# Kernel tuning notes

Measured on AMD Instinct MI355X. Metric: run time of the kernel, lower is better.

## Reference

```python
import jax, jax.numpy as jnp
import numpy as np

NUM_HEADS = 8


def _mha(x, w_in, b_in, w_out, b_out, nh=NUM_HEADS):
    # x: [B, L, H]; torch nn.MultiheadAttention (batch_first) self-attention
    B, L, H = x.shape
    dh = H // nh
    qkv = x @ w_in.T + b_in                      # [B, L, 3H]
    q, k, v = jnp.split(qkv, 3, axis=-1)
    def heads(t):
        return t.reshape(B, L, nh, dh).transpose(0, 2, 1, 3)  # [B, nh, L, dh]
    q, k, v = heads(q), heads(k), heads(v)
    scale = 1.0 / np.sqrt(dh)
    scores = jnp.einsum('bhqd,bhkd->bhqk', q * scale, k)      # [B, nh, L, L]
    attn = jax.nn.softmax(scores, axis=-1)
    out = jnp.einsum('bhqk,bhkd->bhqd', attn, v)               # [B, nh, L, dh]
    out = out.transpose(0, 2, 1, 3).reshape(B, L, H)
    return out @ w_out.T + b_out


def setup_inputs() -> dict:
    key = jax.random.key(0)
    ks = jax.random.split(key, 10)
    S, M, B, H = 64, 4, 128, 1024
    std = 0.02
    inp = {
        'hidden_states_combined': jax.random.normal(ks[0], (S, M, B, 1, H), jnp.float32),
        'mf_in_w': jax.random.normal(ks[1], (3 * H, H), jnp.float32) * std,
        'mf_in_b': jnp.zeros((3 * H,), jnp.float32),
        'mf_out_w': jax.random.normal(ks[2], (H, H), jnp.float32) * std,
        'mf_out_b': jnp.zeros((H,), jnp.float32),
        'sf_in_w': jax.random.normal(ks[3], (3 * H, H), jnp.float32) * std,
        'sf_in_b': jnp.zeros((3 * H,), jnp.float32),
        'sf_out_w': jax.random.normal(ks[4], (H, H), jnp.float32) * std,
        'sf_out_b': jnp.zeros((H,), jnp.float32),
        'pos_enc': jax.random.normal(ks[5], (1, S, H), jnp.float32) * std,
    }
    return inp


def reference(hidden_states_combined, mf_in_w, mf_in_b, mf_out_w, mf_out_b,
              sf_in_w, sf_in_b, sf_out_w, sf_out_b, pos_enc):
    S, M, B, _, H = hidden_states_combined.shape
    # [S, M, B, 1, H] -> [S, B, M, H] -> batch all steps together: [S*B, M, H]
    x = hidden_states_combined[:, :, :, 0, :].transpose(0, 2, 1, 3).reshape(S * B, M, H)
    fused = _mha(x, mf_in_w, mf_in_b, mf_out_w, mf_out_b)        # [S*B, M, H]
    fused = fused.mean(axis=1).reshape(S, B, H)                  # mean over models
    seq = fused.transpose(1, 0, 2) + pos_enc[:, :S, :]            # [B, S, H]
    enhanced = _mha(seq, sf_in_w, sf_in_b, sf_out_w, sf_out_b)   # [B, S, H]
    return enhanced.transpose(1, 0, 2)[:, :, None, :]             # [S, B, 1, H]
```

## Files before the change

### kernel.cpp

```cpp
#include <hip/hip_runtime.h>

typedef unsigned short u16;
typedef __attribute__((ext_vector_type(8))) short bf16x8;
typedef __attribute__((ext_vector_type(4))) float f32x4;

__device__ __forceinline__ u16 f2bf(float f) {
  unsigned u = __float_as_uint(f);
  u += 0x7FFFu + ((u >> 16) & 1u);
  return (u16)(u >> 16);
}
__device__ __forceinline__ float bf2f(u16 h) {
  return __uint_as_float(((unsigned)h) << 16);
}

#define GLOAD16(g, l) __builtin_amdgcn_global_load_lds( \
    (const __attribute__((address_space(1))) void*)(g), \
    (__attribute__((address_space(3))) void*)(l), 16, 0, 0)

__global__ __launch_bounds__(256) void cvtw_kernel(const float* __restrict__ in,
                                                   u16* __restrict__ out, int n4) {
  int i = blockIdx.x * 256 + threadIdx.x;
  if (i >= n4) return;
  float4 f = ((const float4*)in)[i];
  ushort4 u;
  u.x = f2bf(f.x); u.y = f2bf(f.y); u.z = f2bf(f.z); u.w = f2bf(f.w);
  ((ushort4*)out)[i] = u;
}

__global__ __launch_bounds__(256) void xcvt_kernel(const float* __restrict__ hidden,
                                                   u16* __restrict__ xb, int s0) {
  int idx = blockIdx.x * 256 + threadIdx.x;
  int h4 = idx & 255;
  int lrow = idx >> 8;
  int m = lrow & 3;
  int b = (lrow >> 2) & 127;
  int sl = lrow >> 9;
  int s = s0 + sl;
  const float4 f = *(const float4*)(hidden + (((size_t)(s * 4 + m) * 128 + b) * 1024) + h4 * 4);
  ushort4 u;
  u.x = f2bf(f.x); u.y = f2bf(f.y); u.z = f2bf(f.z); u.w = f2bf(f.w);
  *(ushort4*)(xb + (size_t)lrow * 1024 + h4 * 4) = u;
}

template <int MODE>
__global__ __launch_bounds__(256, 2) void gemm_fp(const u16* __restrict__ A,
                                                  const u16* __restrict__ Bw,
                                                  const float* __restrict__ bias,
                                                  void* __restrict__ Cout,
                                                  int N, int K,
                                                  const float* __restrict__ posenc) {
  __shared__ u16 SA[3][8192];
  __shared__ u16 SB[3][4096];
  const int t = threadIdx.x, w = t >> 6, l = t & 63;
  const int lr = l & 15, lg = l >> 4;
  const int wm = w >> 1, wn = w & 1;

  const int gx = gridDim.x;
  const int nb = gx * gridDim.y;
  const int id = blockIdx.y * gx + blockIdx.x;
  const int id2 = (id & 7) * (nb >> 3) + (id >> 3);
  const int rowBase = (id2 / gx) * 256, colBase = (id2 % gx) * 128;

  const int srow = l >> 2;
  const int ssl = ((l & 3) ^ (srow & 3)) * 8;
  const u16* Ag = A + (size_t)(rowBase + w * 16 + srow) * K + ssl;
  const u16* Bg = Bw + (size_t)(colBase + w * 16 + srow) * K + ssl;
  u16* const lA = &SA[0][0] + w * 512;
  u16* const lB = &SB[0][0] + w * 512;

  const int fsw = (lg ^ (lr & 3)) * 8;
  const int aoff = (wm * 128 + lr) * 32 + fsw;
  const int boff = (wn * 64 + lr) * 32 + fsw;

  f32x4 acc[8][4];
#pragma unroll
  for (int i = 0; i < 8; i++)
#pragma unroll
    for (int j = 0; j < 4; j++) acc[i][j] = (f32x4){0.f, 0.f, 0.f, 0.f};

#define STG_P0(tt, bb) do { \
    const size_t ko_ = (size_t)(tt) * 32; \
    GLOAD16(Ag + ko_,                    lA + (bb) * 8192); \
    GLOAD16(Ag + ko_ + (size_t)64 * K,   lA + (bb) * 8192 + 2048); \
    GLOAD16(Ag + ko_ + (size_t)128 * K,  lA + (bb) * 8192 + 4096); \
  } while (0)
#define STG_P1(tt, bb) do { \
    const size_t ko_ = (size_t)(tt) * 32; \
    GLOAD16(Ag + ko_ + (size_t)192 * K,  lA + (bb) * 8192 + 6144); \
    GLOAD16(Bg + ko_,                    lB + (bb) * 4096); \
    GLOAD16(Bg + ko_ + (size_t)64 * K,   lB + (bb) * 4096 + 2048); \
  } while (0)

  const int nt = K >> 5;
  STG_P0(0, 0); STG_P1(0, 0);
  STG_P0(1, 1); STG_P1(1, 1);
  asm volatile("s_waitcnt vmcnt(6)" ::: "memory");
  __builtin_amdgcn_s_barrier();

  int bcur = 0;
  for (int tt = 0; tt < nt; ++tt) {
    const u16* pa = &SA[bcur][0];
    const u16* pb = &SB[bcur][0];
    const int bnext = (bcur + 2 > 2) ? bcur - 1 : bcur + 2;
    bf16x8 af[4], bfr[4];

#pragma unroll
    for (int m = 0; m < 4; m++) af[m] = *(const bf16x8*)(pa + aoff + m * 512);
#pragma unroll
    for (int n = 0; n < 4; n++) bfr[n] = *(const bf16x8*)(pb + boff + n * 512);
    if (tt + 2 < nt) STG_P0(tt + 2, bnext);
    __builtin_amdgcn_s_barrier();
    asm volatile("s_waitcnt lgkmcnt(0)" ::: "memory");
    __builtin_amdgcn_sched_barrier(0);
    __builtin_amdgcn_s_setprio(1);
#pragma unroll
    for (int m = 0; m < 4; m++)
#pragma unroll
      for (int n = 0; n < 4; n++)
        acc[m][n] = __builtin_amdgcn_mfma_f32_16x16x32_bf16(af[m], bfr[n], acc[m][n], 0, 0, 0);
    __builtin_amdgcn_s_setprio(0);
    __builtin_amdgcn_s_barrier();

#pragma unroll
    for (int m = 0; m < 4; m++) af[m] = *(const bf16x8*)(pa + aoff + (m + 4) * 512);
    if (tt + 2 < nt) STG_P1(tt + 2, bnext);
    __builtin_amdgcn_s_barrier();
    asm volatile("s_waitcnt lgkmcnt(0)" ::: "memory");
    __builtin_amdgcn_sched_barrier(0);
    __builtin_amdgcn_s_setprio(1);
#pragma unroll
    for (int m = 0; m < 4; m++)
#pragma unroll
      for (int n = 0; n < 4; n++)
        acc[m + 4][n] = __builtin_amdgcn_mfma_f32_16x16x32_bf16(af[m], bfr[n], acc[m + 4][n], 0, 0, 0);
    __builtin_amdgcn_s_setprio(0);
    if (tt + 2 < nt) {
      asm volatile("s_waitcnt vmcnt(6)" ::: "memory");
    } else if (tt + 1 < nt) {
      asm volatile("s_waitcnt vmcnt(0)" ::: "memory");
    }
    __builtin_amdgcn_s_barrier();
    bcur = (bcur + 1 > 2) ? 0 : bcur + 1;
  }
#undef STG_P0
#undef STG_P1

  const int orow0 = rowBase + wm * 128 + lg * 4;
  const int ocol0 = colBase + wn * 64 + lr;
#pragma unroll
  for (int m = 0; m < 8; m++) {
#pragma unroll
    for (int n = 0; n < 4; n++) {
      const int col = ocol0 + n * 16;
      const float bv = bias[col];
#pragma unroll
      for (int r = 0; r < 4; r++) {
        const int row = orow0 + m * 16 + r;
        float v = acc[m][n][r] + bv;
        if (MODE == 0) {
          ((u16*)Cout)[(size_t)row * N + col] = f2bf(v);
        } else if (MODE == 1) {
          int s = row >> 7, b = row & 127;
          v += posenc[s * 1024 + col];
          ((u16*)Cout)[((size_t)(b * 64 + s)) * 1024 + col] = f2bf(v);
        } else {
          int s = row & 63, b = row >> 6;
          ((float*)Cout)[((size_t)(s * 128 + b)) * 1024 + col] = v;
        }
      }
    }
  }
}

__global__ __launch_bounds__(256) void attn1_kernel(const u16* __restrict__ qkv,
                                                    u16* __restrict__ am, int seqBase) {
  const int w = threadIdx.x >> 6, l = threadIdx.x & 63;
  const int pair = blockIdx.x * 4 + w;
  const int seq = pair >> 3, head = pair & 7;
  const int d0 = l * 2;
  const u16* base = qkv + (size_t)(seq * 4) * 3072 + head * 128 + d0;
  const float scale = 0.08838834764831845f;
  float q[4][2], k[4][2], v[4][2];
#pragma unroll
  for (int m = 0; m < 4; m++) {
    ushort2 uq = *(const ushort2*)(base + (size_t)m * 3072);
    ushort2 uk = *(const ushort2*)(base + (size_t)m * 3072 + 1024);
    ushort2 uv = *(const ushort2*)(base + (size_t)m * 3072 + 2048);
    q[m][0] = bf2f(uq.x) * scale; q[m][1] = bf2f(uq.y) * scale;
    k[m][0] = bf2f(uk.x);         k[m][1] = bf2f(uk.y);
    v[m][0] = bf2f(uv.x);         v[m][1] = bf2f(uv.y);
  }
  float sc[4][4];
#pragma unroll
  for (int i = 0; i < 4; i++)
#pragma unroll
    for (int j = 0; j < 4; j++)
      sc[i][j] = q[i][0] * k[j][0] + q[i][1] * k[j][1];
#pragma unroll
  for (int off = 32; off >= 1; off >>= 1)
#pragma unroll
    for (int i = 0; i < 4; i++)
#pragma unroll
      for (int j = 0; j < 4; j++)
        sc[i][j] += __shfl_xor(sc[i][j], off, 64);
  float pbar[4] = {0.f, 0.f, 0.f, 0.f};
#pragma unroll
  for (int i = 0; i < 4; i++) {
    float mx = fmaxf(fmaxf(sc[i][0], sc[i][1]), fmaxf(sc[i][2], sc[i][3]));
    float e0 = __expf(sc[i][0] - mx), e1 = __expf(sc[i][1] - mx);
    float e2 = __expf(sc[i][2] - mx), e3 = __expf(sc[i][3] - mx);
    float inv = 0.25f / (e0 + e1 + e2 + e3);
    pbar[0] += e0 * inv; pbar[1] += e1 * inv; pbar[2] += e2 * inv; pbar[3] += e3 * inv;
  }
  float o0 = pbar[0] * v[0][0] + pbar[1] * v[1][0] + pbar[2] * v[2][0] + pbar[3] * v[3][0];
  float o1 = pbar[0] * v[0][1] + pbar[1] * v[1][1] + pbar[2] * v[2][1] + pbar[3] * v[3][1];
  ushort2 ou; ou.x = f2bf(o0); ou.y = f2bf(o1);
  *(ushort2*)(am + (size_t)(seqBase + seq) * 1024 + head * 128 + d0) = ou;
}

__global__ __launch_bounds__(256) void attn2_kernel(const u16* __restrict__ qkv2,
                                                    u16* __restrict__ aout) {
  __shared__ u16 Qs[64 * 128];
  __shared__ u16 Ks[64 * 128];
  __shared__ u16 Vt[128 * 72];
  __shared__ u16 Ps[64 * 72];
  const int t = threadIdx.x, w = t >> 6, l = t & 63;
  const int lr = l & 15, lg = l >> 4;
  const int b = blockIdx.x >> 3, head = blockIdx.x & 7;
  const u16* qb = qkv2 + (size_t)(b * 64) * 3072 + head * 128;

#pragma unroll
  for (int c = 0; c < 4; c++) {
    int flat = c * 256 + t;
    int row = flat >> 4, sp = flat & 15;
    int sg = (sp ^ (row & 7)) * 8;
    GLOAD16(qb + (size_t)row * 3072 + sg, Qs + (c * 256 + w * 64) * 8);
    GLOAD16(qb + 1024 + (size_t)row * 3072 + sg, Ks + (c * 256 + w * 64) * 8);
  }
  const int dd = (t & 63) * 2, kb = t >> 6;
#pragma unroll
  for (int c = 0; c < 16; c++) {
    int k = c * 4 + kb;
    ushort2 vv = *(const ushort2*)(qb + 2048 + (size_t)k * 3072 + dd);
    Vt[(size_t)dd * 72 + k] = vv.x;
    Vt[(size_t)(dd + 1) * 72 + k] = vv.y;
  }
  __syncthreads();

  f32x4 sc[4];
#pragma unroll
  for (int cb = 0; cb < 4; cb++) sc[cb] = (f32x4){0.f, 0.f, 0.f, 0.f};
#pragma unroll
  for (int ks = 0; ks < 4; ks++) {
    bf16x8 aq = *(const bf16x8*)(Qs + (w * 16 + lr) * 128 + ((ks * 4 + lg) ^ (lr & 7)) * 8);
#pragma unroll
    for (int cb = 0; cb < 4; cb++) {
      bf16x8 bk = *(const bf16x8*)(Ks + (cb * 16 + lr) * 128 + ((ks * 4 + lg) ^ (lr & 7)) * 8);
      sc[cb] = __builtin_amdgcn_mfma_f32_16x16x32_bf16(aq, bk, sc[cb], 0, 0, 0);
    }
  }

  const float scale = 0.08838834764831845f;
#pragma unroll
  for (int r = 0; r < 4; r++) {
#pragma unroll
    for (int cb = 0; cb < 4; cb++) sc[cb][r] *= scale;
    float mx = fmaxf(fmaxf(sc[0][r], sc[1][r]), fmaxf(sc[2][r], sc[3][r]));
#pragma unroll
    for (int off = 1; off < 16; off <<= 1) mx = fmaxf(mx, __shfl_xor(mx, off, 64));
    float sum = 0.f;
#pragma unroll
    for (int cb = 0; cb < 4; cb++) {
      float e = __expf(sc[cb][r] - mx);
      sum += e;
      sc[cb][r] = e;
    }
#pragma unroll
    for (int off = 1; off < 16; off <<= 1) sum += __shfl_xor(sum, off, 64);
    float inv = 1.f / sum;
    int prow = w * 16 + lg * 4 + r;
#pragma unroll
    for (int cb = 0; cb < 4; cb++)
      Ps[(size_t)prow * 72 + cb * 16 + lr] = f2bf(sc[cb][r] * inv);
  }

  f32x4 o[8];
#pragma unroll
  for (int cb = 0; cb < 8; cb++) o[cb] = (f32x4){0.f, 0.f, 0.f, 0.f};
#pragma unroll
  for (int ks = 0; ks < 2; ks++) {
    bf16x8 ap = *(const bf16x8*)(Ps + (w * 16 + lr) * 72 + ks * 32 + lg * 8);
#pragma unroll
    for (int cb = 0; cb < 8; cb++) {
      bf16x8 bv = *(const bf16x8*)(Vt + (cb * 16 + lr) * 72 + ks * 32 + lg * 8);
      o[cb] = __builtin_amdgcn_mfma_f32_16x16x32_bf16(ap, bv, o[cb], 0, 0, 0);
    }
  }
#pragma unroll
  for (int cb = 0; cb < 8; cb++) {
#pragma unroll
    for (int r = 0; r < 4; r++) {
      int srow = w * 16 + lg * 4 + r;
      int d = cb * 16 + lr;
      aout[(size_t)(b * 64 + srow) * 1024 + head * 128 + d] = f2bf(o[cb][r]);
    }
  }
}

extern "C" void kernel_launch(void* const* d_in, const int* in_sizes, int n_in,
                              void* d_out, int out_size, void* d_ws, size_t ws_size,
                              hipStream_t stream) {
  const float* hidden   = (const float*)d_in[0];
  const float* mf_in_w  = (const float*)d_in[1];
  const float* mf_in_b  = (const float*)d_in[2];
  const float* mf_out_w = (const float*)d_in[3];
  const float* mf_out_b = (const float*)d_in[4];
  const float* sf_in_w  = (const float*)d_in[5];
  const float* sf_in_b  = (const float*)d_in[6];
  const float* sf_out_w = (const float*)d_in[7];
  const float* sf_out_b = (const float*)d_in[8];
  const float* pos_enc  = (const float*)d_in[9];

  char* ws = (char*)d_ws;
  u16* w_mf_in  = (u16*)(ws);
  u16* w_mf_out = (u16*)(ws + 6291456);
  u16* w_sf_in  = (u16*)(ws + 8388608);
  u16* w_sf_out = (u16*)(ws + 14680064);
  u16* xchunk   = (u16*)(ws + 16777216);
  u16* qkvbuf   = (u16*)(ws + 33554432);
  u16* attnmean = (u16*)(ws + 83886080);
  u16* seqbuf   = (u16*)(ws + 100663296);
  u16* a2out    = (u16*)(ws + 117440512);

  cvtw_kernel<<<3072, 256, 0, stream>>>(mf_in_w, w_mf_in, 786432);
  cvtw_kernel<<<1024, 256, 0, stream>>>(mf_out_w, w_mf_out, 262144);
  cvtw_kernel<<<3072, 256, 0, stream>>>(sf_in_w, w_sf_in, 786432);
  cvtw_kernel<<<1024, 256, 0, stream>>>(sf_out_w, w_sf_out, 262144);

  for (int c = 0; c < 4; ++c) {
    xcvt_kernel<<<8192, 256, 0, stream>>>(hidden, xchunk, c * 16);
    gemm_fp<0><<<dim3(24, 32), 256, 0, stream>>>(xchunk, w_mf_in, mf_in_b, qkvbuf,
                                                 3072, 1024, nullptr);
    attn1_kernel<<<4096, 256, 0, stream>>>(qkvbuf, attnmean, c * 2048);
  }

  gemm_fp<1><<<dim3(8, 32), 256, 0, stream>>>(attnmean, w_mf_out, mf_out_b, seqbuf,
                                              1024, 1024, pos_enc);
  gemm_fp<0><<<dim3(24, 32), 256, 0, stream>>>(seqbuf, w_sf_in, sf_in_b, qkvbuf,
                                               3072, 1024, nullptr);
  attn2_kernel<<<1024, 256, 0, stream>>>(qkvbuf, a2out);
  gemm_fp<2><<<dim3(8, 32), 256, 0, stream>>>(a2out, w_sf_out, sf_out_b, d_out,
                                              1024, 1024, nullptr);
}
```

Baseline: 530.2 us.

## Add 256x256 eight-wave pipelined GEMM for QKV projections and unchunk when workspace allows

Adds a new 512-thread GEMM kernel with 256x256 output tiles, a 64 KB LDS double buffer split into K-halves, and fine-grained phases that interleave LDS fragment reads, async global-to-LDS staging and MFMA under raised priority. It replaces the 256x128 GEMM for both in-projection GEMMs. When the workspace is large enough, the first stage also runs over the whole batch in one launch of each kernel instead of four chunks, which cuts launch count and tail effects. The cost is much higher LDS and register pressure per block and a larger workspace requirement.

After: 478.6 us. 9.7% less time.

```diff
diff --git a/kernel.cpp b/kernel.cpp
--- a/kernel.cpp
+++ b/kernel.cpp
@@ -42,6 +42,121 @@
   *(ushort4*)(xb + (size_t)lrow * 1024 + h4 * 4) = u;
 }
 
+template <int KK>
+__global__ __launch_bounds__(512, 2) void gemm8p(const u16* __restrict__ A,
+                                                 const u16* __restrict__ Bw,
+                                                 const float* __restrict__ bias,
+                                                 u16* __restrict__ C, int N) {
+  __shared__ u16 Sh[65536];
+  const int t = threadIdx.x, w = t >> 6, l = t & 63;
+  const int lr = l & 15, lg = l >> 4;
+  const int wm = w >> 2, wn = w & 3;
+
+  const int gx = gridDim.x;
+  const int nb = gx * gridDim.y;
+  const int id = blockIdx.y * gx + blockIdx.x;
+  const int id2 = (id & 7) * (nb >> 3) + (id >> 3);
+  const int rowBase = (id2 / gx) * 256, colBase = (id2 % gx) * 256;
+
+  const int sslot8 = ((t & 3) ^ ((t >> 3) & 3)) * 8;
+  const u16* Ag = A + (size_t)(rowBase + (t >> 2)) * KK + sslot8;
+  const u16* Bg = Bw + (size_t)(colBase + (t >> 2)) * KK + sslot8;
+  const size_t K128 = (size_t)128 * KK;
+  const int ldsW = w * 512;
+
+  const int fslot8 = (lg ^ ((lr >> 1) & 3)) * 8;
+  const int aRowOff = (wm * 128 + lr) * 32 + fslot8;
+  const int bRowOff = (wn * 64 + lr) * 32 + fslot8;
+
+  f32x4 acc[8][4];
+#pragma unroll
+  for (int i = 0; i < 8; i++)
+#pragma unroll
+    for (int j = 0; j < 4; j++) acc[i][j] = (f32x4){0.f, 0.f, 0.f, 0.f};
+  bf16x8 af[4], bfr[4];
+
+#define STGA(tt, KH, DB) { \
+    const u16* g_ = Ag + (size_t)(tt) * 64 + (KH) * 32; \
+    GLOAD16(g_, Sh + ((DB) * 2 + (KH)) * 8192 + ldsW); \
+    GLOAD16(g_ + K128, Sh + ((DB) * 2 + (KH)) * 8192 + 4096 + ldsW); }
+#define STGB(tt, KH, DB) { \
+    const u16* g_ = Bg + (size_t)(tt) * 64 + (KH) * 32; \
+    GLOAD16(g_, Sh + 32768 + ((DB) * 2 + (KH)) * 8192 + ldsW); \
+    GLOAD16(g_ + K128, Sh + 32768 + ((DB) * 2 + (KH)) * 8192 + 4096 + ldsW); }
+
+#define PHASE(DD, KH, MG, DOB, STG, WT) do { \
+    const u16* sa_ = Sh + ((DD) * 2 + (KH)) * 8192 + aRowOff; \
+    _Pragma("unroll") \
+    for (int mi = 0; mi < 4; mi++) af[mi] = *(const bf16x8*)(sa_ + ((MG) * 4 + mi) * 512); \
+    if (DOB) { \
+      const u16* sb_ = Sh + 32768 + ((DD) * 2 + (KH)) * 8192 + bRowOff; \
+      _Pragma("unroll") \
+      for (int n = 0; n < 4; n++) bfr[n] = *(const bf16x8*)(sb_ + n * 512); \
+    } \
+    STG; \
+    __builtin_amdgcn_s_barrier(); \
+    asm volatile("s_waitcnt lgkmcnt(0)" ::: "memory"); \
+    __builtin_amdgcn_sched_barrier(0); \
+    __builtin_amdgcn_s_setprio(1); \
+    _Pragma("unroll") \
+    for (int mi = 0; mi < 4; mi++) { \
+      _Pragma("unroll") \
+      for (int n = 0; n < 4; n++) \
+        acc[(MG) * 4 + mi][n] = \
+            __builtin_amdgcn_mfma_f32_16x16x32_bf16(af[mi], bfr[n], acc[(MG) * 4 + mi][n], 0, 0, 0); \
+    } \
+    __builtin_amdgcn_s_setprio(0); \
+    WT; \
+    __builtin_amdgcn_s_barrier(); \
+  } while (0)
+
+  STGA(0, 0, 0); STGB(0, 0, 0);
+  STGA(0, 1, 0); STGB(0, 1, 0);
+  STGA(1, 0, 1); STGB(1, 0, 1);
+  asm volatile("s_waitcnt vmcnt(4)" ::: "memory");
+  __builtin_amdgcn_s_barrier();
+
+  const int NIT = KK / 128;
+  int t0 = 0;
+  for (int it = 0; it < NIT - 1; ++it, t0 += 2) {
+    PHASE(0, 0, 0, 1, STGA(t0 + 1, 1, 1), );
+    PHASE(0, 0, 1, 0, STGB(t0 + 1, 1, 1), );
+    PHASE(0, 1, 0, 1, STGA(t0 + 2, 0, 0), );
+    PHASE(0, 1, 1, 0, STGB(t0 + 2, 0, 0), asm volatile("s_waitcnt vmcnt(4)" ::: "memory"));
+    PHASE(1, 0, 0, 1, STGA(t0 + 2, 1, 0), );
+    PHASE(1, 0, 1, 0, STGB(t0 + 2, 1, 0), );
+    PHASE(1, 1, 0, 1, STGA(t0 + 3, 0, 1), );
+    PHASE(1, 1, 1, 0, STGB(t0 + 3, 0, 1), asm volatile("s_waitcnt vmcnt(4)" ::: "memory"));
+  }
+  PHASE(0, 0, 0, 1, STGA(t0 + 1, 1, 1), );
+  PHASE(0, 0, 1, 0, STGB(t0 + 1, 1, 1), );
+  PHASE(0, 1, 0, 1, , );
+  PHASE(0, 1, 1, 0, , asm volatile("s_waitcnt vmcnt(0)" ::: "memory"));
+  PHASE(1, 0, 0, 1, , );
+  PHASE(1, 0, 1, 0, , );
+  PHASE(1, 1, 0, 1, , );
+  PHASE(1, 1, 1, 0, , );
+#undef PHASE
+#undef STGA
+#undef STGB
+
+  const int orow0 = rowBase + wm * 128 + lg * 4;
+  const int ocol0 = colBase + wn * 64 + lr;
+#pragma unroll
+  for (int m = 0; m < 8; m++) {
+#pragma unroll
+    for (int n = 0; n < 4; n++) {
+      const int col = ocol0 + n * 16;
+      const float bv = bias[col];
+#pragma unroll
+      for (int r = 0; r < 4; r++) {
+        const int row = orow0 + m * 16 + r;
+        C[(size_t)row * N + col] = f2bf(acc[m][n][r] + bv);
+      }
+    }
+  }
+}
+
 template <int MODE>
 __global__ __launch_bounds__(256, 2) void gemm_fp(const u16* __restrict__ A,
                                                   const u16* __restrict__ Bw,
@@ -157,9 +272,7 @@
       for (int r = 0; r < 4; r++) {
         const int row = orow0 + m * 16 + r;
         float v = acc[m][n][r] + bv;
-        if (MODE == 0) {
-          ((u16*)Cout)[(size_t)row * N + col] = f2bf(v);
-        } else if (MODE == 1) {
+        if (MODE == 1) {
           int s = row >> 7, b = row & 127;
           v += posenc[s * 1024 + col];
           ((u16*)Cout)[((size_t)(b * 64 + s)) * 1024 + col] = f2bf(v);
@@ -326,29 +439,47 @@
   u16* w_mf_out = (u16*)(ws + 6291456);
   u16* w_sf_in  = (u16*)(ws + 8388608);
   u16* w_sf_out = (u16*)(ws + 14680064);
-  u16* xchunk   = (u16*)(ws + 16777216);
-  u16* qkvbuf   = (u16*)(ws + 33554432);
-  u16* attnmean = (u16*)(ws + 83886080);
-  u16* seqbuf   = (u16*)(ws + 100663296);
-  u16* a2out    = (u16*)(ws + 117440512);
 
   cvtw_kernel<<<3072, 256, 0, stream>>>(mf_in_w, w_mf_in, 786432);
   cvtw_kernel<<<1024, 256, 0, stream>>>(mf_out_w, w_mf_out, 262144);
   cvtw_kernel<<<3072, 256, 0, stream>>>(sf_in_w, w_sf_in, 786432);
   cvtw_kernel<<<1024, 256, 0, stream>>>(sf_out_w, w_sf_out, 262144);
 
-  for (int c = 0; c < 4; ++c) {
-    xcvt_kernel<<<8192, 256, 0, stream>>>(hidden, xchunk, c * 16);
-    gemm_fp<0><<<dim3(24, 32), 256, 0, stream>>>(xchunk, w_mf_in, mf_in_b, qkvbuf,
-                                                 3072, 1024, nullptr);
-    attn1_kernel<<<4096, 256, 0, stream>>>(qkvbuf, attnmean, c * 2048);
-  }
-
-  gemm_fp<1><<<dim3(8, 32), 256, 0, stream>>>(attnmean, w_mf_out, mf_out_b, seqbuf,
-                                              1024, 1024, pos_enc);
-  gemm_fp<0><<<dim3(24, 32), 256, 0, stream>>>(seqbuf, w_sf_in, sf_in_b, qkvbuf,
-                                               3072, 1024, nullptr);
-  attn2_kernel<<<1024, 256, 0, stream>>>(qkvbuf, a2out);
-  gemm_fp<2><<<dim3(8, 32), 256, 0, stream>>>(a2out, w_sf_out, sf_out_b, d_out,
-                                              1024, 1024, nullptr);
-}
+  if (ws_size >= 335544320ull) {
+    u16* xfull    = (u16*)(ws + 16777216);
+    u16* qkvfull  = (u16*)(ws + 83886080);
+    u16* attnmean = (u16*)(ws + 285212672);
+    u16* seqbuf   = (u16*)(ws + 301989888);
+    u16* a2out    = (u16*)(ws + 318767104);
+
+    xcvt_kernel<<<32768, 256, 0, stream>>>(hidden, xfull, 0);
+    gemm8p<1024><<<dim3(12, 128), 512, 0, stream>>>(xfull, w_mf_in, mf_in_b, qkvfull, 3072);
+    attn1_kernel<<<16384, 256, 0, stream>>>(qkvfull, attnmean, 0);
+
+    gemm_fp<1><<<dim3(8, 32), 256, 0, stream>>>(attnmean, w_mf_out, mf_out_b, seqbuf,
+                                                1024, 1024, pos_enc);
+    gemm8p<1024><<<dim3(12, 32), 512, 0, stream>>>(seqbuf, w_sf_in, sf_in_b, qkvfull, 3072);
+    attn2_kernel<<<1024, 256, 0, stream>>>(qkvfull, a2out);
+    gemm_fp<2><<<dim3(8, 32), 256, 0, stream>>>(a2out, w_sf_out, sf_out_b, d_out,
+                                                1024, 1024, nullptr);
+  } else {
+    u16* xchunk   = (u16*)(ws + 16777216);
+    u16* qkvbuf   = (u16*)(ws + 33554432);
+    u16* attnmean = (u16*)(ws + 83886080);
+    u16* seqbuf   = (u16*)(ws + 100663296);
+    u16* a2out    = (u16*)(ws + 117440512);
+
+    for (int c = 0; c < 4; ++c) {
+      xcvt_kernel<<<8192, 256, 0, stream>>>(hidden, xchunk, c * 16);
+      gemm8p<1024><<<dim3(12, 32), 512, 0, stream>>>(xchunk, w_mf_in, mf_in_b, qkvbuf, 3072);
+      attn1_kernel<<<4096, 256, 0, stream>>>(qkvbuf, attnmean, c * 2048);
+    }
+
+    gemm_fp<1><<<dim3(8, 32), 256, 0, stream>>>(attnmean, w_mf_out, mf_out_b, seqbuf,
+                                                1024, 1024, pos_enc);
+    gemm8p<1024><<<dim3(12, 32), 512, 0, stream>>>(seqbuf, w_sf_in, sf_in_b, qkvbuf, 3072);
+    attn2_kernel<<<1024, 256, 0, stream>>>(qkvbuf, a2out);
+    gemm_fp<2><<<dim3(8, 32), 256, 0, stream>>>(a2out, w_sf_out, sf_out_b, d_out,
+                                                1024, 1024, nullptr);
+  }
+}
```

## Restructure GEMM k-loop barriers and launch full-batch pipeline when workspace allows

Applied to the files above, without the earlier changes.

The GEMM inner loop now issues both halves of the A-fragment LDS reads and both global-to-LDS prefetch stages up front. It uses partial lgkmcnt waits instead of two extra workgroup barriers per k-step, so MFMA work can overlap outstanding LDS reads. Separately, when the workspace is large enough, the first attention stage runs as one large conversion, GEMM and attention launch over all 64 steps instead of four chunks. This cuts launch count and tail effects but needs a much larger workspace. Holding a second A fragment set raises register pressure, and dropping the mid-iteration barriers relies on the triple-buffer spacing staying correct.

Result: faster. 512.8 us (-3.3%).

```diff
diff --git a/kernel.cpp b/kernel.cpp
--- a/kernel.cpp
+++ b/kernel.cpp
@@ -43,7 +43,7 @@
 }
 
 template <int MODE>
-__global__ __launch_bounds__(256, 2) void gemm_fp(const u16* __restrict__ A,
+__global__ __launch_bounds__(256, 2) void gemm_r3(const u16* __restrict__ A,
                                                   const u16* __restrict__ Bw,
                                                   const float* __restrict__ bias,
                                                   void* __restrict__ Cout,
@@ -90,11 +90,14 @@
     GLOAD16(Bg + ko_,                    lB + (bb) * 4096); \
     GLOAD16(Bg + ko_ + (size_t)64 * K,   lB + (bb) * 4096 + 2048); \
   } while (0)
+#define LG(NN) asm volatile("s_waitcnt lgkmcnt(" #NN ")" ::: "memory"); \
+               __builtin_amdgcn_sched_barrier(0)
+#define WTC(NN) asm volatile("s_waitcnt vmcnt(" #NN ")" ::: "memory")
 
   const int nt = K >> 5;
   STG_P0(0, 0); STG_P1(0, 0);
   STG_P0(1, 1); STG_P1(1, 1);
-  asm volatile("s_waitcnt vmcnt(6)" ::: "memory");
+  WTC(6);
   __builtin_amdgcn_s_barrier();
 
   int bcur = 0;
@@ -102,16 +105,18 @@
     const u16* pa = &SA[bcur][0];
     const u16* pb = &SB[bcur][0];
     const int bnext = (bcur + 2 > 2) ? bcur - 1 : bcur + 2;
-    bf16x8 af[4], bfr[4];
+    bf16x8 af[4], ag[4], bfr[4];
 
 #pragma unroll
     for (int m = 0; m < 4; m++) af[m] = *(const bf16x8*)(pa + aoff + m * 512);
 #pragma unroll
     for (int n = 0; n < 4; n++) bfr[n] = *(const bf16x8*)(pb + boff + n * 512);
     if (tt + 2 < nt) STG_P0(tt + 2, bnext);
-    __builtin_amdgcn_s_barrier();
-    asm volatile("s_waitcnt lgkmcnt(0)" ::: "memory");
-    __builtin_amdgcn_sched_barrier(0);
+#pragma unroll
+    for (int m = 0; m < 4; m++) ag[m] = *(const bf16x8*)(pa + aoff + (m + 4) * 512);
+    if (tt + 2 < nt) STG_P1(tt + 2, bnext);
+
+    LG(4);
     __builtin_amdgcn_s_setprio(1);
 #pragma unroll
     for (int m = 0; m < 4; m++)
@@ -119,31 +124,27 @@
       for (int n = 0; n < 4; n++)
         acc[m][n] = __builtin_amdgcn_mfma_f32_16x16x32_bf16(af[m], bfr[n], acc[m][n], 0, 0, 0);
     __builtin_amdgcn_s_setprio(0);
-    __builtin_amdgcn_s_barrier();
-
-#pragma unroll
-    for (int m = 0; m < 4; m++) af[m] = *(const bf16x8*)(pa + aoff + (m + 4) * 512);
-    if (tt + 2 < nt) STG_P1(tt + 2, bnext);
-    __builtin_amdgcn_s_barrier();
-    asm volatile("s_waitcnt lgkmcnt(0)" ::: "memory");
-    __builtin_amdgcn_sched_barrier(0);
+    LG(0);
     __builtin_amdgcn_s_setprio(1);
 #pragma unroll
     for (int m = 0; m < 4; m++)
 #pragma unroll
       for (int n = 0; n < 4; n++)
-        acc[m + 4][n] = __builtin_amdgcn_mfma_f32_16x16x32_bf16(af[m], bfr[n], acc[m + 4][n], 0, 0, 0);
+        acc[m + 4][n] = __builtin_amdgcn_mfma_f32_16x16x32_bf16(ag[m], bfr[n], acc[m + 4][n], 0, 0, 0);
     __builtin_amdgcn_s_setprio(0);
+
     if (tt + 2 < nt) {
-      asm volatile("s_waitcnt vmcnt(6)" ::: "memory");
+      WTC(6);
     } else if (tt + 1 < nt) {
-      asm volatile("s_waitcnt vmcnt(0)" ::: "memory");
+      WTC(0);
     }
     __builtin_amdgcn_s_barrier();
     bcur = (bcur + 1 > 2) ? 0 : bcur + 1;
   }
+#undef WTC
+#undef LG
+#undef STG_P1
 #undef STG_P0
-#undef STG_P1
 
   const int orow0 = rowBase + wm * 128 + lg * 4;
   const int ocol0 = colBase + wn * 64 + lr;
@@ -326,29 +327,51 @@
   u16* w_mf_out = (u16*)(ws + 6291456);
   u16* w_sf_in  = (u16*)(ws + 8388608);
   u16* w_sf_out = (u16*)(ws + 14680064);
-  u16* xchunk   = (u16*)(ws + 16777216);
-  u16* qkvbuf   = (u16*)(ws + 33554432);
-  u16* attnmean = (u16*)(ws + 83886080);
-  u16* seqbuf   = (u16*)(ws + 100663296);
-  u16* a2out    = (u16*)(ws + 117440512);
 
   cvtw_kernel<<<3072, 256, 0, stream>>>(mf_in_w, w_mf_in, 786432);
   cvtw_kernel<<<1024, 256, 0, stream>>>(mf_out_w, w_mf_out, 262144);
   cvtw_kernel<<<3072, 256, 0, stream>>>(sf_in_w, w_sf_in, 786432);
   cvtw_kernel<<<1024, 256, 0, stream>>>(sf_out_w, w_sf_out, 262144);
 
-  for (int c = 0; c < 4; ++c) {
-    xcvt_kernel<<<8192, 256, 0, stream>>>(hidden, xchunk, c * 16);
-    gemm_fp<0><<<dim3(24, 32), 256, 0, stream>>>(xchunk, w_mf_in, mf_in_b, qkvbuf,
+  if (ws_size >= 335544320ull) {
+    u16* xfull    = (u16*)(ws + 16777216);
+    u16* qkvfull  = (u16*)(ws + 83886080);
+    u16* attnmean = (u16*)(ws + 285212672);
+    u16* seqbuf   = (u16*)(ws + 301989888);
+    u16* a2out    = (u16*)(ws + 318767104);
+
+    xcvt_kernel<<<32768, 256, 0, stream>>>(hidden, xfull, 0);
+    gemm_r3<0><<<dim3(24, 128), 256, 0, stream>>>(xfull, w_mf_in, mf_in_b, qkvfull,
+                                                  3072, 1024, nullptr);
+    attn1_kernel<<<16384, 256, 0, stream>>>(qkvfull, attnmean, 0);
+
+    gemm_r3<1><<<dim3(8, 32), 256, 0, stream>>>(attnmean, w_mf_out, mf_out_b, seqbuf,
+                                                1024, 1024, pos_enc);
+    gemm_r3<0><<<dim3(24, 32), 256, 0, stream>>>(seqbuf, w_sf_in, sf_in_b, qkvfull,
                                                  3072, 1024, nullptr);
-    attn1_kernel<<<4096, 256, 0, stream>>>(qkvbuf, attnmean, c * 2048);
-  }
-
-  gemm_fp<1><<<dim3(8, 32), 256, 0, stream>>>(attnmean, w_mf_out, mf_out_b, seqbuf,
-                                              1024, 1024, pos_enc);
-  gemm_fp<0><<<dim3(24, 32), 256, 0, stream>>>(seqbuf, w_sf_in, sf_in_b, qkvbuf,
-                                               3072, 1024, nullptr);
-  attn2_kernel<<<1024, 256, 0, stream>>>(qkvbuf, a2out);
-  gemm_fp<2><<<dim3(8, 32), 256, 0, stream>>>(a2out, w_sf_out, sf_out_b, d_out,
-                                              1024, 1024, nullptr);
-}
+    attn2_kernel<<<1024, 256, 0, stream>>>(qkvfull, a2out);
+    gemm_r3<2><<<dim3(8, 32), 256, 0, stream>>>(a2out, w_sf_out, sf_out_b, d_out,
+                                                1024, 1024, nullptr);
+  } else {
+    u16* xchunk   = (u16*)(ws + 16777216);
+    u16* qkvbuf   = (u16*)(ws + 33554432);
+    u16* attnmean = (u16*)(ws + 83886080);
+    u16* seqbuf   = (u16*)(ws + 100663296);
+    u16* a2out    = (u16*)(ws + 117440512);
+
+    for (int c = 0; c < 4; ++c) {
+      xcvt_kernel<<<8192, 256, 0, stream>>>(hidden, xchunk, c * 16);
+      gemm_r3<0><<<dim3(24, 32), 256, 0, stream>>>(xchunk, w_mf_in, mf_in_b, qkvbuf,
+                                                   3072, 1024, nullptr);
+      attn1_kernel<<<4096, 256, 0, stream>>>(qkvbuf, attnmean, c * 2048);
+    }
+
+    gemm_r3<1><<<dim3(8, 32), 256, 0, stream>>>(attnmean, w_mf_out, mf_out_b, seqbuf,
+                                                1024, 1024, pos_enc);
+    gemm_r3<0><<<dim3(24, 32), 256, 0, stream>>>(seqbuf, w_sf_in, sf_in_b, qkvbuf,
+                                                 3072, 1024, nullptr);
+    attn2_kernel<<<1024, 256, 0, stream>>>(qkvbuf, a2out);
+    gemm_r3<2><<<dim3(8, 32), 256, 0, stream>>>(a2out, w_sf_out, sf_out_b, d_out,
+                                                1024, 1024, nullptr);
+  }
+}
```
